# Kernel optimization log

Hardware: AMD Instinct MI355X
Metric: run time of the kernel (lower is better)

Reference implementation:

```python
import jax, jax.numpy as jnp
import numpy as np

NUM_HEADS = 16
THETA = 10000.0


def _rope(x, pos, theta):
    # x: [B, H, S, D], pos: [S] ints. Interleaved-pair RoPE.
    D = x.shape[-1]
    half = D // 2
    inv_freq = theta ** (-(jnp.arange(half, dtype=jnp.float32) * 2.0) / D)  # [half]
    ang = pos.astype(jnp.float32)[:, None] * inv_freq[None, :]              # [S, half]
    cos, sin = jnp.cos(ang), jnp.sin(ang)
    x1 = x[..., 0::2]
    x2 = x[..., 1::2]
    r1 = x1 * cos - x2 * sin
    r2 = x1 * sin + x2 * cos
    return jnp.stack([r1, r2], axis=-1).reshape(x.shape)


def setup_inputs() -> dict:
    key = jax.random.key(0)
    ks = jax.random.split(key, 5)
    B, S, D = 4, 2048, 1024
    scale = 1.0 / np.sqrt(D)
    x = jax.random.normal(ks[0], (B, S, D), dtype=jnp.float32)
    Wq = jax.random.normal(ks[1], (D, D), dtype=jnp.float32) * scale
    Wk = jax.random.normal(ks[2], (D, D), dtype=jnp.float32) * scale
    Wv = jax.random.normal(ks[3], (D, D), dtype=jnp.float32) * scale
    Wo = jax.random.normal(ks[4], (D, D), dtype=jnp.float32) * scale
    token_positions = jnp.arange(S, dtype=jnp.int64)
    return {"x": x, "Wq": Wq, "Wk": Wk, "Wv": Wv, "Wo": Wo,
            "token_positions": token_positions}


def reference(x, Wq, Wk, Wv, Wo, token_positions):
    B, S, D = x.shape
    H = NUM_HEADS
    hd = D // H
    # Projections (weights stored as [d_model, d_k], matching the transposed params)
    q = jnp.einsum('bsd,de->bse', x, Wq).reshape(B, S, H, hd).transpose(0, 2, 1, 3)
    k = jnp.einsum('bsd,de->bse', x, Wk).reshape(B, S, H, hd).transpose(0, 2, 1, 3)
    v = jnp.einsum('bsd,de->bse', x, Wv).reshape(B, S, H, hd).transpose(0, 2, 1, 3)
    # RoPE on q and k
    q = _rope(q, token_positions, THETA)
    k = _rope(k, token_positions, THETA)
    # Causal scaled dot-product attention
    scores = jnp.einsum('bhqd,bhkd->bhqk', q, k) / jnp.sqrt(jnp.float32(hd))
    causal = jnp.tril(jnp.ones((S, S), dtype=bool))
    scores = jnp.where(causal, scores, jnp.float32(-jnp.inf))
    attn = jax.nn.softmax(scores, axis=-1)
    o = jnp.einsum('bhqk,bhkd->bhqd', attn, v)          # [B, H, S, hd]
    o = o.transpose(0, 2, 1, 3).reshape(B, S, D)         # [B, S, D]
    return jnp.einsum('bsd,de->bse', o, Wo)
```

## Files before the change

kernel.cpp:

```cpp
#include <hip/hip_runtime.h>
#include <math.h>

#define B_ 4
#define S_ 2048
#define D_ 1024
#define H_ 16
#define HD_ 64
#define ES_F 0.180336880111f
#define KF (-0.41524101186f)

typedef unsigned short ushort_t;
typedef __attribute__((ext_vector_type(8))) short short8;
typedef __attribute__((ext_vector_type(4))) short short4_t;
typedef __attribute__((ext_vector_type(4))) float f32x4;
typedef __attribute__((ext_vector_type(16))) float f32x16;
typedef __attribute__((ext_vector_type(2))) unsigned uint2v;

typedef const void __attribute__((address_space(1))) gvoid;
typedef void __attribute__((address_space(3))) lvoid;

__device__ __forceinline__ ushort_t f2bf(float f) {
    union { float f; unsigned u; } v; v.f = f;
    unsigned r = (v.u + 0x7FFFu + ((v.u >> 16) & 1u)) >> 16;
    return (ushort_t)r;
}
__device__ __forceinline__ float fexp2(float x) {
#if __has_builtin(__builtin_amdgcn_exp2f)
    return __builtin_amdgcn_exp2f(x);
#else
    return exp2f(x);
#endif
}
__device__ __forceinline__ unsigned pk2t(float a, float b) {
    union { float f; unsigned u; } A, Bv; A.f = a; Bv.f = b;
#if __has_builtin(__builtin_amdgcn_perm)
    return __builtin_amdgcn_perm(Bv.u, A.u, 0x07060302u);
#else
    return (A.u >> 16) | (Bv.u & 0xFFFF0000u);
#endif
}
__device__ __forceinline__ short8 mk_frag(unsigned a, unsigned b, unsigned c, unsigned d) {
    union { unsigned u[4]; short8 s; } t;
    t.u[0] = a; t.u[1] = b; t.u[2] = c; t.u[3] = d; return t.s;
}

__global__ __launch_bounds__(256)
void cvt_all(const float* __restrict__ x, ushort_t* __restrict__ xb,
             const float* __restrict__ W0, const float* __restrict__ W1,
             const float* __restrict__ W2, const float* __restrict__ W3,
             ushort_t* __restrict__ T0, ushort_t* __restrict__ T1,
             ushort_t* __restrict__ T2, ushort_t* __restrict__ T3)
{
    __shared__ __align__(16) float T[64 * 68];
    const int bx = blockIdx.x;
    const int t = threadIdx.x;

    if (bx < 4096) {
        const size_t i = ((size_t)bx * 256 + t) * 8;
        float4 a = *(const float4*)&x[i];
        float4 b = *(const float4*)&x[i + 4];
        short8 o;
        o[0] = (short)f2bf(a.x); o[1] = (short)f2bf(a.y);
        o[2] = (short)f2bf(a.z); o[3] = (short)f2bf(a.w);
        o[4] = (short)f2bf(b.x); o[5] = (short)f2bf(b.y);
        o[6] = (short)f2bf(b.z); o[7] = (short)f2bf(b.w);
        *(short8*)&xb[i] = o;
        return;
    }

    const int id = bx - 4096;
    const int z = id >> 8;
    const float* W = (z == 0) ? W0 : (z == 1) ? W1 : (z == 2) ? W2 : W3;
    ushort_t* Wt = (z == 0) ? T0 : (z == 1) ? T1 : (z == 2) ? T2 : T3;
    const int n0 = (id & 15) * 64, k0 = ((id >> 4) & 15) * 64;

    const int row = t >> 2, c0 = (t & 3) * 16;
#pragma unroll
    for (int u = 0; u < 4; ++u)
        *(float4*)&T[row * 68 + c0 + u * 4] =
            *(const float4*)&W[(size_t)(k0 + row) * D_ + n0 + c0 + u * 4];
    __syncthreads();
    const int n = t >> 2, kc = (t & 3) * 16;
    short8 o0, o1;
#pragma unroll
    for (int kk = 0; kk < 8; ++kk) o0[kk] = (short)f2bf(T[(kc + kk) * 68 + n]);
#pragma unroll
    for (int kk = 0; kk < 8; ++kk) o1[kk] = (short)f2bf(T[(kc + 8 + kk) * 68 + n]);
    *(short8*)&Wt[(size_t)(n0 + n) * D_ + k0 + kc] = o0;
    *(short8*)&Wt[(size_t)(n0 + n) * D_ + k0 + kc + 8] = o1;
}


#define STAGE(tt, Ad, Bd) {                                                    \
    const int kk_ = (tt) * 64;                                                 \
    _Pragma("unroll") for (int i_ = 0; i_ < 4; ++i_) {                         \
        const int rb_ = (i_ * 4 + w) * 8;                                      \
        __builtin_amdgcn_global_load_lds(                                      \
            (gvoid*)&pA[(size_t)(aBase + rb_ + srow) * D_ + kk_ + sch],        \
            (lvoid*)&(Ad)[rb_ * 64], 16, 0, 0);                                \
        __builtin_amdgcn_global_load_lds(                                      \
            (gvoid*)&pB[(size_t)(bBase + rb_ + srow) * D_ + kk_ + sch],        \
            (lvoid*)&(Bd)[rb_ * 64], 16, 0, 0);                                \
    } }

#define COMPUTE(Ab, Bb) {                                                      \
    _Pragma("unroll") for (int ks = 0; ks < 4; ++ks) {                         \
        const int xr_ = (((ks * 2 + hl) ^ (lq & 7)) << 3);                     \
        short8 af0 = *(const short8*)&(Ab)[(wr * 64 + lq) * 64 + xr_];         \
        short8 af1 = *(const short8*)&(Ab)[(wr * 64 + 32 + lq) * 64 + xr_];    \
        short8 bf0 = *(const short8*)&(Bb)[(wc * 64 + lq) * 64 + xr_];         \
        short8 bf1 = *(const short8*)&(Bb)[(wc * 64 + 32 + lq) * 64 + xr_];    \
        acc[0][0] = __builtin_amdgcn_mfma_f32_32x32x16_bf16(af0, bf0, acc[0][0], 0, 0, 0); \
        acc[0][1] = __builtin_amdgcn_mfma_f32_32x32x16_bf16(af0, bf1, acc[0][1], 0, 0, 0); \
        acc[1][0] = __builtin_amdgcn_mfma_f32_32x32x16_bf16(af1, bf0, acc[1][0], 0, 0, 0); \
        acc[1][1] = __builtin_amdgcn_mfma_f32_32x32x16_bf16(af1, bf1, acc[1][1], 0, 0, 0); \
    } }

__global__ __launch_bounds__(256, 2)
void gemm_bt(const ushort_t* __restrict__ A,
             const ushort_t* __restrict__ W0, const ushort_t* __restrict__ W1,
             const ushort_t* __restrict__ W2,
             void* __restrict__ d0, void* __restrict__ d1, void* __restrict__ d2,
             const int mode_base)
{
    __shared__ __align__(16) ushort_t As[2 * 128 * 64];
    __shared__ __align__(16) ushort_t Bs[2 * 128 * 64];

    const int tid = threadIdx.x;
    const int lane = tid & 63;
    const int hl = lane >> 5;
    const int lq = lane & 31;
    const int w = tid >> 6, wr = w >> 1, wc = w & 1;
    const int z = blockIdx.z;
    const ushort_t* Wt = (z == 0) ? W0 : (z == 1) ? W1 : W2;
    const int mode = mode_base + z;
    const bool sw = (mode == 0) || (mode == 1);

    const int tokT = blockIdx.x * 128, featT = blockIdx.y * 128;
    const ushort_t* pA = sw ? Wt : A;
    const ushort_t* pB = sw ? A : Wt;
    const int aBase = sw ? featT : tokT;
    const int bBase = sw ? tokT : featT;

    const f32x16 zv16 = {0,0,0,0,0,0,0,0,0,0,0,0,0,0,0,0};
    f32x16 acc[2][2];
    acc[0][0] = zv16; acc[0][1] = zv16; acc[1][0] = zv16; acc[1][1] = zv16;

    const int srow = lane >> 3;
    const int spc  = lane & 7;
    const int sch  = (spc ^ srow) * 8;

    ushort_t* A0 = As;  ushort_t* A1 = As + 128 * 64;
    ushort_t* B0 = Bs;  ushort_t* B1 = Bs + 128 * 64;

    STAGE(0, A0, B0);
    __syncthreads();

#pragma unroll 1
    for (int t2 = 0; t2 < 8; ++t2) {
        STAGE(2 * t2 + 1, A1, B1);
        COMPUTE(A0, B0);
        __syncthreads();
        if (t2 < 7) STAGE(2 * t2 + 2, A0, B0);
        COMPUTE(A1, B1);
        __syncthreads();
    }

    if (mode == 2) {
#pragma unroll
        for (int tn = 0; tn < 2; ++tn) {
            const int n = bBase + wc * 64 + tn * 32 + lq;
            const int h = n >> 6, dd = n & 63;
#pragma unroll
            for (int tm = 0; tm < 2; ++tm) {
                const int mb = aBase + wr * 64 + tm * 32 + 4 * hl;
#pragma unroll
                for (int g = 0; g < 4; ++g) {
                    const int m_base = mb + 8 * g;
                    const int bb2 = m_base >> 11, s0 = m_base & (S_ - 1);
                    short4_t pk;
#pragma unroll
                    for (int r = 0; r < 4; ++r)
                        pk[r] = (short)f2bf(acc[tm][tn][4 * g + r]);
                    *(short4_t*)&((ushort_t*)d2)[(((size_t)bb2 * H_ + h) * HD_ + dd) * S_ + s0] = pk;
                }
            }
        }
    } else if (mode == 3) {
        float* outp = (float*)d0;
#pragma unroll
        for (int tn = 0; tn < 2; ++tn) {
            const int n = bBase + wc * 64 + tn * 32 + lq;
#pragma unroll
            for (int tm = 0; tm < 2; ++tm) {
                const int mb = aBase + wr * 64 + tm * 32 + 4 * hl;
#pragma unroll
                for (int g = 0; g < 4; ++g)
#pragma unroll
                    for (int r = 0; r < 4; ++r)
                        outp[(size_t)(mb + 8 * g + r) * D_ + n] =
                            acc[tm][tn][4 * g + r];
            }
        }
    } else {
        ushort_t* dst = (mode == 0) ? (ushort_t*)d0 : (ushort_t*)d1;
        const float sc = (mode == 0) ? ES_F : 1.0f;
#pragma unroll
        for (int tn = 0; tn < 2; ++tn) {
            const int tok = bBase + wc * 64 + tn * 32 + lq;
            const int bb2 = tok >> 11, s0 = tok & (S_ - 1);
            const float fs0 = (float)s0;
#pragma unroll
            for (int tm = 0; tm < 2; ++tm) {
                const int fb = aBase + wr * 64 + tm * 32 + 4 * hl;
                const int h = fb >> 6;
                const int ddb = fb & 63;
                ushort_t* dp = &dst[(((size_t)bb2 * H_ + h) * S_ + s0) * HD_];
#pragma unroll
                for (int g = 0; g < 4; ++g) {
                    const int dd = ddb + 8 * g;
                    const int jj = dd >> 1;
                    const float if0 = exp2f(KF * (float)jj);
                    const float if1 = exp2f(KF * (float)(jj + 1));
                    float sn0, cs0, sn1, cs1;
                    __sincosf(fs0 * if0, &sn0, &cs0);
                    __sincosf(fs0 * if1, &sn1, &cs1);
                    const float x0 = acc[tm][tn][4 * g + 0];
                    const float x1 = acc[tm][tn][4 * g + 1];
                    const float x2 = acc[tm][tn][4 * g + 2];
                    const float x3 = acc[tm][tn][4 * g + 3];
                    short4_t pk;
                    pk[0] = (short)f2bf((x0 * cs0 - x1 * sn0) * sc);
                    pk[1] = (short)f2bf((x0 * sn0 + x1 * cs0) * sc);
                    pk[2] = (short)f2bf((x2 * cs1 - x3 * sn1) * sc);
                    pk[3] = (short)f2bf((x2 * sn1 + x3 * cs1) * sc);
                    *(short4_t*)&dp[dd] = pk;
                }
            }
        }
    }
}

__global__ __launch_bounds__(256)
void attn_mfma(const ushort_t* __restrict__ Q, const ushort_t* __restrict__ K,
               const ushort_t* __restrict__ Vt, ushort_t* __restrict__ O)
{
    __shared__ __align__(16) ushort_t sK[64 * 64];
    __shared__ __align__(16) ushort_t sVt[64 * 64];

    const int tid = threadIdx.x;
    const int lane = tid & 63;
    const int hl = lane >> 5;
    const int lq = lane & 31;
    const int w = tid >> 6;
    const int hb64 = blockIdx.x;
    const int pair = blockIdx.y;
    const int h = hb64 >> 2, bb = hb64 & 3;
    const size_t hb = ((size_t)(bb * H_ + h)) * S_ * HD_;

    const int srow = lane >> 3;
    const int spc = lane & 7;

    const f32x16 zv16 = {0,0,0,0,0,0,0,0,0,0,0,0,0,0,0,0};

    for (int pass = 0; pass < 2; ++pass) {
        const int q0 = ((pass == 0) ? (15 - pair) : pair) * 128;
        const int wq = q0 + w * 32;
        const int qg = wq + lq;

        short8 qf[4];
#pragma unroll
        for (int ks = 0; ks < 4; ++ks)
            qf[ks] = *(const short8*)&Q[hb + (size_t)qg * HD_ + ks * 16 + hl * 8];

        f32x16 oa[2];
        oa[0] = zv16; oa[1] = zv16;
        float ls = 0.f;

        const int nt = q0 / 64 + 2;
        for (int kt = 0; kt < nt; ++kt) {
            const int k0 = kt * 64;
            __syncthreads();
            {
#pragma unroll
                for (int i = 0; i < 2; ++i) {
                    const int row = i * 32 + w * 8 + srow;
                    const int sc = (spc ^ (row & 7)) * 8;
                    __builtin_amdgcn_global_load_lds(
                        (gvoid*)&K[hb + (size_t)(k0 + row) * HD_ + sc],
                        (lvoid*)&sK[(i * 32 + w * 8) * 64], 16, 0, 0);
                    __builtin_amdgcn_global_load_lds(
                        (gvoid*)&Vt[hb + (size_t)row * S_ + k0 + sc],
                        (lvoid*)&sVt[(i * 32 + w * 8) * 64], 16, 0, 0);
                }
            }
            __syncthreads();

            if (k0 > wq + 31) continue;

            f32x16 st[2];
            st[0] = zv16; st[1] = zv16;
            const int kr0 = lq, kr1 = 32 + lq;
#pragma unroll
            for (int ks = 0; ks < 4; ++ks) {
                const int ch = ks * 2 + hl;
                short8 ak0 = *(const short8*)&sK[kr0 * 64 + ((ch ^ (kr0 & 7)) << 3)];
                short8 ak1 = *(const short8*)&sK[kr1 * 64 + ((ch ^ (kr1 & 7)) << 3)];
                st[0] = __builtin_amdgcn_mfma_f32_32x32x16_bf16(ak0, qf[ks], st[0], 0, 0, 0);
                st[1] = __builtin_amdgcn_mfma_f32_32x32x16_bf16(ak1, qf[ks], st[1], 0, 0, 0);
            }

            const bool diag = (k0 + 63 > wq);
            short8 pf[4];
#pragma unroll
            for (int nt2 = 0; nt2 < 2; ++nt2) {
                float pv[16];
                const int kb = k0 + nt2 * 32 + 4 * hl;
#pragma unroll
                for (int g = 0; g < 4; ++g)
#pragma unroll
                    for (int r = 0; r < 4; ++r) {
                        float s = st[nt2][4 * g + r];
                        if (diag) {
                            const int key = kb + 8 * g + r;
                            s = (key <= qg) ? s : -INFINITY;
                        }
                        pv[4 * g + r] = fexp2(s);
                    }
#pragma unroll
                for (int m = 0; m < 16; ++m) {
                    union { float f; unsigned u; } tv; tv.f = pv[m];
                    tv.u &= 0xFFFF0000u;
                    ls += tv.f;
                }
                unsigned P2[8];
#pragma unroll
                for (int g = 0; g < 4; ++g) {
                    P2[2 * g]     = pk2t(pv[4 * g + 0], pv[4 * g + 1]);
                    P2[2 * g + 1] = pk2t(pv[4 * g + 2], pv[4 * g + 3]);
                }
#if __has_builtin(__builtin_amdgcn_permlane32_swap)
                uint2v r02 = __builtin_amdgcn_permlane32_swap(P2[0], P2[2], false, false);
                uint2v r13 = __builtin_amdgcn_permlane32_swap(P2[1], P2[3], false, false);
                uint2v r46 = __builtin_amdgcn_permlane32_swap(P2[4], P2[6], false, false);
                uint2v r57 = __builtin_amdgcn_permlane32_swap(P2[5], P2[7], false, false);
                pf[nt2 * 2 + 0] = mk_frag(r02[0], r13[0], r02[1], r13[1]);
                pf[nt2 * 2 + 1] = mk_frag(r46[0], r57[0], r46[1], r57[1]);
#else
                unsigned X[8];
#pragma unroll
                for (int m = 0; m < 8; ++m) X[m] = (unsigned)__shfl_xor((int)P2[m], 32);
                pf[nt2 * 2 + 0] = hl ? mk_frag(X[2], X[3], P2[2], P2[3])
                                     : mk_frag(P2[0], P2[1], X[0], X[1]);
                pf[nt2 * 2 + 1] = hl ? mk_frag(X[6], X[7], P2[6], P2[7])
                                     : mk_frag(P2[4], P2[5], X[4], X[5]);
#endif
            }

            const int vr0 = lq, vr1 = 32 + lq;
#pragma unroll
            for (int ks2 = 0; ks2 < 4; ++ks2) {
                const int ch = ks2 * 2 + hl;
                short8 av0 = *(const short8*)&sVt[vr0 * 64 + ((ch ^ (vr0 & 7)) << 3)];
                short8 av1 = *(const short8*)&sVt[vr1 * 64 + ((ch ^ (vr1 & 7)) << 3)];
                oa[0] = __builtin_amdgcn_mfma_f32_32x32x16_bf16(av0, pf[ks2], oa[0], 0, 0, 0);
                oa[1] = __builtin_amdgcn_mfma_f32_32x32x16_bf16(av1, pf[ks2], oa[1], 0, 0, 0);
            }
        }

        const float lsum = ls + __shfl_xor(ls, 32);
        const float inv = 1.f / lsum;
        ushort_t* Ob = &O[((size_t)(bb * S_ + qg)) * D_ + h * HD_];
#pragma unroll
        for (int mt = 0; mt < 2; ++mt)
#pragma unroll
            for (int g = 0; g < 4; ++g) {
                short4_t pk;
#pragma unroll
                for (int r = 0; r < 4; ++r)
                    pk[r] = (short)f2bf(oa[mt][4 * g + r] * inv);
                *(short4_t*)&Ob[mt * 32 + 8 * g + 4 * hl] = pk;
            }
    }
}

extern "C" void kernel_launch(void* const* d_in, const int* in_sizes, int n_in,
                              void* d_out, int out_size, void* d_ws, size_t ws_size,
                              hipStream_t stream)
{
    (void)in_sizes; (void)n_in; (void)out_size; (void)ws_size;
    const float* x  = (const float*)d_in[0];
    const float* Wq = (const float*)d_in[1];
    const float* Wk = (const float*)d_in[2];
    const float* Wv = (const float*)d_in[3];
    const float* Wo = (const float*)d_in[4];

    float* out = (float*)d_out;
    ushort_t* ws = (ushort_t*)d_ws;
    const size_t NX = (size_t)B_ * S_ * D_;
    const size_t NW = (size_t)D_ * D_;
    ushort_t* xb  = ws;
    ushort_t* Wqt = xb + NX;
    ushort_t* Wkt = Wqt + NW;
    ushort_t* Wvt = Wkt + NW;
    ushort_t* Wot = Wvt + NW;
    ushort_t* Qb  = Wot + NW;
    ushort_t* Kb  = Qb + NX;
    ushort_t* Vtb = Kb + NX;
    ushort_t* Ob  = Vtb + NX;

    cvt_all<<<dim3(4096 + 1024), 256, 0, stream>>>(x, xb, Wq, Wk, Wv, Wo,
                                                   Wqt, Wkt, Wvt, Wot);

    gemm_bt<<<dim3(64, 8, 3), 256, 0, stream>>>(xb, Wqt, Wkt, Wvt, Qb, Kb, Vtb, 0);
    attn_mfma<<<dim3(64, 8), 256, 0, stream>>>(Qb, Kb, Vtb, Ob);
    gemm_bt<<<dim3(64, 8, 1), 256, 0, stream>>>(Ob, Wot, Wot, Wot, out, nullptr, nullptr, 3);
}
```

Measured before the change: 254.6 us.

## Fuse Q/K/V projections into one kernel sharing the staged x tile

Replaces the three-way z-batched QKV GEMM with a single fused kernel. Each block loads one x tile and the matching Wq/Wk/Wv tiles, then computes all three projections, so x is read once instead of three times. The kernel is single-buffered with two barriers per k-step, where the old GEMM was double-buffered. It holds three sets of accumulators, which raises register pressure and may lower occupancy. Grid size drops from 1536 to 512 blocks, and the output GEMM is simplified to a dedicated fp32-output path.

New measurement: 247.0 us. 1.03x faster.

```diff
diff --git a/kernel.cpp b/kernel.cpp
--- a/kernel.cpp
+++ b/kernel.cpp
@@ -88,6 +88,156 @@
     for (int kk = 0; kk < 8; ++kk) o1[kk] = (short)f2bf(T[(kc + 8 + kk) * 68 + n]);
     *(short8*)&Wt[(size_t)(n0 + n) * D_ + k0 + kc] = o0;
     *(short8*)&Wt[(size_t)(n0 + n) * D_ + k0 + kc + 8] = o1;
+}
+
+
+#define QSTAGE(tt, src, base, dst) {                                           \
+    const int kk_ = (tt) * 64;                                                 \
+    _Pragma("unroll") for (int i_ = 0; i_ < 4; ++i_) {                         \
+        const int rb_ = (i_ * 4 + w) * 8;                                      \
+        __builtin_amdgcn_global_load_lds(                                      \
+            (gvoid*)&(src)[(size_t)((base) + rb_ + srow) * D_ + kk_ + sch],    \
+            (lvoid*)&(dst)[rb_ * 64], 16, 0, 0);                               \
+    } }
+
+__global__ __launch_bounds__(256, 2)
+void qkv_fused(const ushort_t* __restrict__ A,
+               const ushort_t* __restrict__ Wq, const ushort_t* __restrict__ Wk,
+               const ushort_t* __restrict__ Wv,
+               ushort_t* __restrict__ dQ, ushort_t* __restrict__ dK,
+               ushort_t* __restrict__ dV)
+{
+    __shared__ __align__(16) ushort_t Xs[128 * 64];
+    __shared__ __align__(16) ushort_t Qs[128 * 64];
+    __shared__ __align__(16) ushort_t Ks[128 * 64];
+    __shared__ __align__(16) ushort_t Vs[128 * 64];
+
+    const int tid = threadIdx.x;
+    const int lane = tid & 63;
+    const int hl = lane >> 5;
+    const int lq = lane & 31;
+    const int w = tid >> 6;
+    const int th = w & 1;
+    const int fh = w >> 1;
+
+    const int tokT = blockIdx.x * 128, featT = blockIdx.y * 128;
+
+    const f32x16 zv16 = {0,0,0,0,0,0,0,0,0,0,0,0,0,0,0,0};
+    f32x16 accQ[2][2], accK[2][2], accV[2][2];
+#pragma unroll
+    for (int a = 0; a < 2; ++a)
+#pragma unroll
+        for (int b = 0; b < 2; ++b) {
+            accQ[a][b] = zv16; accK[a][b] = zv16; accV[a][b] = zv16;
+        }
+
+    const int srow = lane >> 3;
+    const int spc  = lane & 7;
+    const int sch  = (spc ^ srow) * 8;
+
+#pragma unroll 1
+    for (int t = 0; t < 16; ++t) {
+        __syncthreads();
+        QSTAGE(t, A,  tokT,  Xs);
+        QSTAGE(t, Wq, featT, Qs);
+        QSTAGE(t, Wk, featT, Ks);
+        QSTAGE(t, Wv, featT, Vs);
+        __syncthreads();
+
+#pragma unroll
+        for (int ks = 0; ks < 4; ++ks) {
+            const int xr = (((ks * 2 + hl) ^ (lq & 7)) << 3);
+            short8 xf0 = *(const short8*)&Xs[(th * 64 + lq) * 64 + xr];
+            short8 xf1 = *(const short8*)&Xs[(th * 64 + 32 + lq) * 64 + xr];
+            short8 qf0 = *(const short8*)&Qs[(fh * 64 + lq) * 64 + xr];
+            short8 qf1 = *(const short8*)&Qs[(fh * 64 + 32 + lq) * 64 + xr];
+            short8 kf0 = *(const short8*)&Ks[(fh * 64 + lq) * 64 + xr];
+            short8 kf1 = *(const short8*)&Ks[(fh * 64 + 32 + lq) * 64 + xr];
+            short8 vf0 = *(const short8*)&Vs[(fh * 64 + lq) * 64 + xr];
+            short8 vf1 = *(const short8*)&Vs[(fh * 64 + 32 + lq) * 64 + xr];
+            accQ[0][0] = __builtin_amdgcn_mfma_f32_32x32x16_bf16(qf0, xf0, accQ[0][0], 0, 0, 0);
+            accQ[0][1] = __builtin_amdgcn_mfma_f32_32x32x16_bf16(qf0, xf1, accQ[0][1], 0, 0, 0);
+            accQ[1][0] = __builtin_amdgcn_mfma_f32_32x32x16_bf16(qf1, xf0, accQ[1][0], 0, 0, 0);
+            accQ[1][1] = __builtin_amdgcn_mfma_f32_32x32x16_bf16(qf1, xf1, accQ[1][1], 0, 0, 0);
+            accK[0][0] = __builtin_amdgcn_mfma_f32_32x32x16_bf16(kf0, xf0, accK[0][0], 0, 0, 0);
+            accK[0][1] = __builtin_amdgcn_mfma_f32_32x32x16_bf16(kf0, xf1, accK[0][1], 0, 0, 0);
+            accK[1][0] = __builtin_amdgcn_mfma_f32_32x32x16_bf16(kf1, xf0, accK[1][0], 0, 0, 0);
+            accK[1][1] = __builtin_amdgcn_mfma_f32_32x32x16_bf16(kf1, xf1, accK[1][1], 0, 0, 0);
+            accV[0][0] = __builtin_amdgcn_mfma_f32_32x32x16_bf16(xf0, vf0, accV[0][0], 0, 0, 0);
+            accV[0][1] = __builtin_amdgcn_mfma_f32_32x32x16_bf16(xf0, vf1, accV[0][1], 0, 0, 0);
+            accV[1][0] = __builtin_amdgcn_mfma_f32_32x32x16_bf16(xf1, vf0, accV[1][0], 0, 0, 0);
+            accV[1][1] = __builtin_amdgcn_mfma_f32_32x32x16_bf16(xf1, vf1, accV[1][1], 0, 0, 0);
+        }
+    }
+
+#pragma unroll
+    for (int tn = 0; tn < 2; ++tn) {
+        const int tok = tokT + th * 64 + tn * 32 + lq;
+        const int bb2 = tok >> 11, s0 = tok & (S_ - 1);
+        const float fs0 = (float)s0;
+#pragma unroll
+        for (int tm = 0; tm < 2; ++tm) {
+            const int fb = featT + fh * 64 + tm * 32 + 4 * hl;
+            const int h = fb >> 6;
+            const int ddb = fb & 63;
+            ushort_t* dpQ = &dQ[(((size_t)bb2 * H_ + h) * S_ + s0) * HD_];
+            ushort_t* dpK = &dK[(((size_t)bb2 * H_ + h) * S_ + s0) * HD_];
+#pragma unroll
+            for (int g = 0; g < 4; ++g) {
+                const int dd = ddb + 8 * g;
+                const int jj = dd >> 1;
+                const float if0 = exp2f(KF * (float)jj);
+                const float if1 = exp2f(KF * (float)(jj + 1));
+                float sn0, cs0, sn1, cs1;
+                __sincosf(fs0 * if0, &sn0, &cs0);
+                __sincosf(fs0 * if1, &sn1, &cs1);
+                {
+                    const float x0 = accQ[tm][tn][4 * g + 0];
+                    const float x1 = accQ[tm][tn][4 * g + 1];
+                    const float x2 = accQ[tm][tn][4 * g + 2];
+                    const float x3 = accQ[tm][tn][4 * g + 3];
+                    short4_t pk;
+                    pk[0] = (short)f2bf((x0 * cs0 - x1 * sn0) * ES_F);
+                    pk[1] = (short)f2bf((x0 * sn0 + x1 * cs0) * ES_F);
+                    pk[2] = (short)f2bf((x2 * cs1 - x3 * sn1) * ES_F);
+                    pk[3] = (short)f2bf((x2 * sn1 + x3 * cs1) * ES_F);
+                    *(short4_t*)&dpQ[dd] = pk;
+                }
+                {
+                    const float x0 = accK[tm][tn][4 * g + 0];
+                    const float x1 = accK[tm][tn][4 * g + 1];
+                    const float x2 = accK[tm][tn][4 * g + 2];
+                    const float x3 = accK[tm][tn][4 * g + 3];
+                    short4_t pk;
+                    pk[0] = (short)f2bf(x0 * cs0 - x1 * sn0);
+                    pk[1] = (short)f2bf(x0 * sn0 + x1 * cs0);
+                    pk[2] = (short)f2bf(x2 * cs1 - x3 * sn1);
+                    pk[3] = (short)f2bf(x2 * sn1 + x3 * cs1);
+                    *(short4_t*)&dpK[dd] = pk;
+                }
+            }
+        }
+    }
+
+#pragma unroll
+    for (int tn = 0; tn < 2; ++tn) {
+        const int n = featT + fh * 64 + tn * 32 + lq;
+        const int h = n >> 6, dd = n & 63;
+#pragma unroll
+        for (int tm = 0; tm < 2; ++tm) {
+            const int mb = tokT + th * 64 + tm * 32 + 4 * hl;
+#pragma unroll
+            for (int g = 0; g < 4; ++g) {
+                const int m_base = mb + 8 * g;
+                const int bb2 = m_base >> 11, s0 = m_base & (S_ - 1);
+                short4_t pk;
+#pragma unroll
+                for (int r = 0; r < 4; ++r)
+                    pk[r] = (short)f2bf(accV[tm][tn][4 * g + r]);
+                *(short4_t*)&dV[(((size_t)bb2 * H_ + h) * HD_ + dd) * S_ + s0] = pk;
+            }
+        }
+    }
 }
 
 
@@ -117,11 +267,8 @@
     } }
 
 __global__ __launch_bounds__(256, 2)
-void gemm_bt(const ushort_t* __restrict__ A,
-             const ushort_t* __restrict__ W0, const ushort_t* __restrict__ W1,
-             const ushort_t* __restrict__ W2,
-             void* __restrict__ d0, void* __restrict__ d1, void* __restrict__ d2,
-             const int mode_base)
+void gemm_bt(const ushort_t* __restrict__ A, const ushort_t* __restrict__ W0,
+             float* __restrict__ outp)
 {
     __shared__ __align__(16) ushort_t As[2 * 128 * 64];
     __shared__ __align__(16) ushort_t Bs[2 * 128 * 64];
@@ -131,16 +278,12 @@
     const int hl = lane >> 5;
     const int lq = lane & 31;
     const int w = tid >> 6, wr = w >> 1, wc = w & 1;
-    const int z = blockIdx.z;
-    const ushort_t* Wt = (z == 0) ? W0 : (z == 1) ? W1 : W2;
-    const int mode = mode_base + z;
-    const bool sw = (mode == 0) || (mode == 1);
 
     const int tokT = blockIdx.x * 128, featT = blockIdx.y * 128;
-    const ushort_t* pA = sw ? Wt : A;
-    const ushort_t* pB = sw ? A : Wt;
-    const int aBase = sw ? featT : tokT;
-    const int bBase = sw ? tokT : featT;
+    const ushort_t* pA = A;
+    const ushort_t* pB = W0;
+    const int aBase = tokT;
+    const int bBase = featT;
 
     const f32x16 zv16 = {0,0,0,0,0,0,0,0,0,0,0,0,0,0,0,0};
     f32x16 acc[2][2];
@@ -166,77 +309,18 @@
         __syncthreads();
     }
 
-    if (mode == 2) {
-#pragma unroll
-        for (int tn = 0; tn < 2; ++tn) {
-            const int n = bBase + wc * 64 + tn * 32 + lq;
-            const int h = n >> 6, dd = n & 63;
-#pragma unroll
-            for (int tm = 0; tm < 2; ++tm) {
-                const int mb = aBase + wr * 64 + tm * 32 + 4 * hl;
-#pragma unroll
-                for (int g = 0; g < 4; ++g) {
-                    const int m_base = mb + 8 * g;
-                    const int bb2 = m_base >> 11, s0 = m_base & (S_ - 1);
-                    short4_t pk;
-#pragma unroll
-                    for (int r = 0; r < 4; ++r)
-                        pk[r] = (short)f2bf(acc[tm][tn][4 * g + r]);
-                    *(short4_t*)&((ushort_t*)d2)[(((size_t)bb2 * H_ + h) * HD_ + dd) * S_ + s0] = pk;
-                }
-            }
-        }
-    } else if (mode == 3) {
-        float* outp = (float*)d0;
-#pragma unroll
-        for (int tn = 0; tn < 2; ++tn) {
-            const int n = bBase + wc * 64 + tn * 32 + lq;
-#pragma unroll
-            for (int tm = 0; tm < 2; ++tm) {
-                const int mb = aBase + wr * 64 + tm * 32 + 4 * hl;
-#pragma unroll
-                for (int g = 0; g < 4; ++g)
-#pragma unroll
-                    for (int r = 0; r < 4; ++r)
-                        outp[(size_t)(mb + 8 * g + r) * D_ + n] =
-                            acc[tm][tn][4 * g + r];
-            }
-        }
-    } else {
-        ushort_t* dst = (mode == 0) ? (ushort_t*)d0 : (ushort_t*)d1;
-        const float sc = (mode == 0) ? ES_F : 1.0f;
-#pragma unroll
-        for (int tn = 0; tn < 2; ++tn) {
-            const int tok = bBase + wc * 64 + tn * 32 + lq;
-            const int bb2 = tok >> 11, s0 = tok & (S_ - 1);
-            const float fs0 = (float)s0;
-#pragma unroll
-            for (int tm = 0; tm < 2; ++tm) {
-                const int fb = aBase + wr * 64 + tm * 32 + 4 * hl;
-                const int h = fb >> 6;
-                const int ddb = fb & 63;
-                ushort_t* dp = &dst[(((size_t)bb2 * H_ + h) * S_ + s0) * HD_];
-#pragma unroll
-                for (int g = 0; g < 4; ++g) {
-                    const int dd = ddb + 8 * g;
-                    const int jj = dd >> 1;
-                    const float if0 = exp2f(KF * (float)jj);
-                    const float if1 = exp2f(KF * (float)(jj + 1));
-                    float sn0, cs0, sn1, cs1;
-                    __sincosf(fs0 * if0, &sn0, &cs0);
-                    __sincosf(fs0 * if1, &sn1, &cs1);
-                    const float x0 = acc[tm][tn][4 * g + 0];
-                    const float x1 = acc[tm][tn][4 * g + 1];
-                    const float x2 = acc[tm][tn][4 * g + 2];
-                    const float x3 = acc[tm][tn][4 * g + 3];
-                    short4_t pk;
-                    pk[0] = (short)f2bf((x0 * cs0 - x1 * sn0) * sc);
-                    pk[1] = (short)f2bf((x0 * sn0 + x1 * cs0) * sc);
-                    pk[2] = (short)f2bf((x2 * cs1 - x3 * sn1) * sc);
-                    pk[3] = (short)f2bf((x2 * sn1 + x3 * cs1) * sc);
-                    *(short4_t*)&dp[dd] = pk;
-                }
-            }
+#pragma unroll
+    for (int tn = 0; tn < 2; ++tn) {
+        const int n = bBase + wc * 64 + tn * 32 + lq;
+#pragma unroll
+        for (int tm = 0; tm < 2; ++tm) {
+            const int mb = aBase + wr * 64 + tm * 32 + 4 * hl;
+#pragma unroll
+            for (int g = 0; g < 4; ++g)
+#pragma unroll
+                for (int r = 0; r < 4; ++r)
+                    outp[(size_t)(mb + 8 * g + r) * D_ + n] =
+                        acc[tm][tn][4 * g + r];
         }
     }
 }
@@ -412,7 +496,7 @@
     cvt_all<<<dim3(4096 + 1024), 256, 0, stream>>>(x, xb, Wq, Wk, Wv, Wo,
                                                    Wqt, Wkt, Wvt, Wot);
 
-    gemm_bt<<<dim3(64, 8, 3), 256, 0, stream>>>(xb, Wqt, Wkt, Wvt, Qb, Kb, Vtb, 0);
+    qkv_fused<<<dim3(64, 8), 256, 0, stream>>>(xb, Wqt, Wkt, Wvt, Qb, Kb, Vtb);
     attn_mfma<<<dim3(64, 8), 256, 0, stream>>>(Qb, Kb, Vtb, Ob);
-    gemm_bt<<<dim3(64, 8, 1), 256, 0, stream>>>(Ob, Wot, Wot, Wot, out, nullptr, nullptr, 3);
-}
+    gemm_bt<<<dim3(64, 8), 256, 0, stream>>>(Ob, Wot, out);
+}
```
